# Kernel tuning notes

Hardware: AMD Instinct MI355X
Metric: run time of the kernel (lower is better)

The kernel has to match this reference:

```python
import jax, jax.numpy as jnp
import numpy as np

N = 12288
D = 16


def setup_inputs() -> dict:
    key = jax.random.key(0)
    k_a, k_u1, k_u2 = jax.random.split(key, 3)
    # 0/1 directed adjacency matrix (dense, as nx.to_numpy_array produces)
    A = jax.random.randint(k_a, (N, N), 0, 2).astype(jnp.float32)
    # tf.random.uniform init for the factor matrices
    U1 = jax.random.uniform(k_u1, (N, D), dtype=jnp.float32)
    U2 = jax.random.uniform(k_u2, (N, D), dtype=jnp.float32)
    lmbd1 = jnp.float32(0.01)
    return {"A": A, "U1": U1, "U2": U2, "lmbd1": lmbd1}


def reference(A, U1, U2, lmbd1):
    # scores[i,j] = <U1[i], U2[j]>  -> full N x N materialization (hot path)
    scores = U1 @ U2.T  # [N, N]
    # original: log(1 / (1 + exp(-scores))) == log_sigmoid(scores)
    loss = -jnp.sum(A * jax.nn.log_sigmoid(scores))
    # L1 regularization: sum over lmbd1*(|U1| + |U2|) elementwise
    loss = loss + lmbd1 * (jnp.sum(jnp.abs(U1)) + jnp.sum(jnp.abs(U2)))
    return loss
```

## Files before the change

### kernel.cpp

```cpp
#include <hip/hip_runtime.h>

#define N_DIM 12288
#define D_DIM 16
#define TILE  256
#define NTILE (N_DIM / TILE)

typedef float f4 __attribute__((ext_vector_type(4)));

__global__ void zero_kernel(float* __restrict__ out) {
    out[0] = 0.0f;
}

__global__ void l1_kernel(const float* __restrict__ U1,
                          const float* __restrict__ U2,
                          const float* __restrict__ lmbd,
                          float* __restrict__ out) {
    const int M = N_DIM * D_DIM;
    int idx = blockIdx.x * blockDim.x + threadIdx.x;
    int stride = gridDim.x * blockDim.x;
    float s = 0.0f;
    for (int i = idx; i < M; i += stride)
        s += fabsf(U1[i]) + fabsf(U2[i]);
    #pragma unroll
    for (int off = 32; off; off >>= 1)
        s += __shfl_down(s, off, 64);
    __shared__ float ws[4];
    int lane = threadIdx.x & 63;
    int wave = threadIdx.x >> 6;
    if (lane == 0) ws[wave] = s;
    __syncthreads();
    if (threadIdx.x == 0)
        atomicAdd(out, lmbd[0] * (ws[0] + ws[1] + ws[2] + ws[3]));
}

__global__ __launch_bounds__(256, 4)
void loss_kernel(const float* __restrict__ A,
                 const float* __restrict__ U1,
                 const float* __restrict__ U2,
                 float* __restrict__ ws) {
    const int t    = threadIdx.x;
    const int lane = t & 63;
    const int wave = t >> 6;
    const int r0   = blockIdx.y * TILE;
    const int c0   = blockIdx.x * TILE;

    float u2r[4][D_DIM];
    #pragma unroll
    for (int c = 0; c < 4; ++c) {
        const f4* p = (const f4*)(U2 + (size_t)(c0 + lane * 4 + c) * D_DIM);
        f4 qa = p[0], qb = p[1], qc = p[2], qd = p[3];
        u2r[c][0]  = qa.x; u2r[c][1]  = qa.y; u2r[c][2]  = qa.z; u2r[c][3]  = qa.w;
        u2r[c][4]  = qb.x; u2r[c][5]  = qb.y; u2r[c][6]  = qb.z; u2r[c][7]  = qb.w;
        u2r[c][8]  = qc.x; u2r[c][9]  = qc.y; u2r[c][10] = qc.z; u2r[c][11] = qc.w;
        u2r[c][12] = qd.x; u2r[c][13] = qd.y; u2r[c][14] = qd.z; u2r[c][15] = qd.w;
    }

    const int urow0 = __builtin_amdgcn_readfirstlane(r0 + wave * 64);
    const float* __restrict__ up = U1 + (size_t)urow0 * D_DIM;
    const float* __restrict__ ap =
        A + (size_t)(r0 + wave * 64) * N_DIM + (size_t)c0 + lane * 4;

    const float L2E = 1.4426950408889634f;
    float acc = 0.0f;

    f4 av[2], bv[2];

#define LOADG(buf, g)                                                          \
    { buf[0] = *(const f4*)(ap + (size_t)(2 * (g))     * N_DIM);               \
      buf[1] = *(const f4*)(ap + (size_t)(2 * (g) + 1) * N_DIM); }

#define COMPG(buf, g)                                                          \
    { float p0 = 1.0f, p1 = 1.0f, p2 = 1.0f, p3 = 1.0f;                        \
      _Pragma("unroll")                                                        \
      for (int r2 = 0; r2 < 2; ++r2) {                                         \
          const float* u = up + (size_t)(2 * (g) + r2) * D_DIM;                \
          float s0 = 0.f, s1 = 0.f, s2 = 0.f, s3 = 0.f;                        \
          _Pragma("unroll")                                                    \
          for (int k = 0; k < D_DIM; ++k) {                                    \
              float uk = u[k];                    \
              s0 = fmaf(uk, u2r[0][k], s0);                                    \
              s1 = fmaf(uk, u2r[1][k], s1);                                    \
              s2 = fmaf(uk, u2r[2][k], s2);                                    \
              s3 = fmaf(uk, u2r[3][k], s3);                                    \
          }                                                                    \
          float e0 = __builtin_amdgcn_exp2f(-L2E * s0);                        \
          float e1 = __builtin_amdgcn_exp2f(-L2E * s1);                        \
          float e2 = __builtin_amdgcn_exp2f(-L2E * s2);                        \
          float e3 = __builtin_amdgcn_exp2f(-L2E * s3);                        \
          f4 a = buf[r2];                                                      \
          p0 *= fmaf(a.x, e0, 1.0f);                                           \
          p1 *= fmaf(a.y, e1, 1.0f);                                           \
          p2 *= fmaf(a.z, e2, 1.0f);                                           \
          p3 *= fmaf(a.w, e3, 1.0f);                                           \
      }                                                                        \
      acc += __builtin_amdgcn_logf((p0 * p1) * (p2 * p3)); }

    LOADG(av, 0);
    #pragma unroll
    for (int gg = 0; gg < 16; ++gg) {
        LOADG(bv, 2 * gg + 1);
        COMPG(av, 2 * gg);
        if (gg < 15) LOADG(av, 2 * gg + 2);
        COMPG(bv, 2 * gg + 1);
    }
#undef LOADG
#undef COMPG

    float part = acc * 0.69314718055994531f;

    #pragma unroll
    for (int off = 32; off; off >>= 1)
        part += __shfl_down(part, off, 64);
    __shared__ float wsum[4];
    if (lane == 0) wsum[wave] = part;
    __syncthreads();
    if (t == 0)
        ws[blockIdx.y * NTILE + blockIdx.x] =
            wsum[0] + wsum[1] + wsum[2] + wsum[3];
}

__global__ void reduce_kernel(const float* __restrict__ ws,
                              float* __restrict__ out) {
    const int M = NTILE * NTILE;
    float s = 0.0f;
    for (int i = threadIdx.x; i < M; i += 256)
        s += ws[i];
    #pragma unroll
    for (int off = 32; off; off >>= 1)
        s += __shfl_down(s, off, 64);
    __shared__ float wsum[4];
    int lane = threadIdx.x & 63;
    int wave = threadIdx.x >> 6;
    if (lane == 0) wsum[wave] = s;
    __syncthreads();
    if (threadIdx.x == 0)
        atomicAdd(out, wsum[0] + wsum[1] + wsum[2] + wsum[3]);
}

extern "C" void kernel_launch(void* const* d_in, const int* in_sizes, int n_in,
                              void* d_out, int out_size, void* d_ws, size_t ws_size,
                              hipStream_t stream) {
    const float* A    = (const float*)d_in[0];
    const float* U1   = (const float*)d_in[1];
    const float* U2   = (const float*)d_in[2];
    const float* lmbd = (const float*)d_in[3];
    float* out = (float*)d_out;
    float* wsf = (float*)d_ws;

    zero_kernel<<<1, 64, 0, stream>>>(out);
    l1_kernel<<<256, 256, 0, stream>>>(U1, U2, lmbd, out);

    dim3 grid(NTILE, NTILE);
    loss_kernel<<<grid, 256, 0, stream>>>(A, U1, U2, wsf);
    reduce_kernel<<<1, 256, 0, stream>>>(wsf, out);
}
```

Baseline: 780.2 us.

## Pack adjacency matrix into a bitmap before the fused loss kernel

Adds a pre-pass that turns the float adjacency matrix into a 1-bit-per-entry bitmap by testing one exponent bit of each float. The loss kernel then stages its 256x256 bit tile in shared memory and decodes A per element, instead of streaming float4 loads through a software double buffer. The full A matrix is still read once per call, by the pack kernel, so this adds an extra launch and an 18 MB write and read-back. It also assumes every A entry is exactly 0.0 or 1.0, and the main loop is now only partially unrolled.

```diff
diff --git a/kernel.cpp b/kernel.cpp
--- a/kernel.cpp
+++ b/kernel.cpp
@@ -4,6 +4,8 @@
 #define D_DIM 16
 #define TILE  256
 #define NTILE (N_DIM / TILE)
+#define BM_BYTES ((size_t)N_DIM * N_DIM / 8)
+#define PART_OFF (32u << 20)
 
 typedef float f4 __attribute__((ext_vector_type(4)));
 
@@ -33,16 +35,42 @@
         atomicAdd(out, lmbd[0] * (ws[0] + ws[1] + ws[2] + ws[3]));
 }
 
+__global__ __launch_bounds__(256, 8)
+void pack_kernel(const float* __restrict__ A, unsigned char* __restrict__ bm) {
+    size_t idx = (size_t)blockIdx.x * blockDim.x + threadIdx.x;
+    size_t stride = (size_t)gridDim.x * blockDim.x;
+    #pragma unroll 4
+    for (size_t b = idx; b < BM_BYTES; b += stride) {
+        const uint4* p = (const uint4*)(A + b * 8);
+        uint4 x = p[0], y = p[1];
+        unsigned v =  ((x.x >> 29) & 1u)        | (((x.y >> 29) & 1u) << 1)
+                   | (((x.z >> 29) & 1u) << 2)  | (((x.w >> 29) & 1u) << 3)
+                   | (((y.x >> 29) & 1u) << 4)  | (((y.y >> 29) & 1u) << 5)
+                   | (((y.z >> 29) & 1u) << 6)  | (((y.w >> 29) & 1u) << 7);
+        bm[b] = (unsigned char)v;
+    }
+}
+
 __global__ __launch_bounds__(256, 4)
-void loss_kernel(const float* __restrict__ A,
+void loss_kernel(const unsigned char* __restrict__ bm,
                  const float* __restrict__ U1,
                  const float* __restrict__ U2,
-                 float* __restrict__ ws) {
+                 float* __restrict__ partials) {
     const int t    = threadIdx.x;
     const int lane = t & 63;
     const int wave = t >> 6;
     const int r0   = blockIdx.y * TILE;
     const int c0   = blockIdx.x * TILE;
+
+    __shared__ unsigned char bmt[TILE * (TILE / 8)];
+
+    {
+        const uint4* src = (const uint4*)(bm + (size_t)(r0 + t) * (N_DIM / 8)
+                                             + (size_t)(c0 / 8));
+        uint4* dst = (uint4*)(bmt + t * 32);
+        dst[0] = src[0];
+        dst[1] = src[1];
+    }
 
     float u2r[4][D_DIM];
     #pragma unroll
@@ -55,56 +83,47 @@
         u2r[c][12] = qd.x; u2r[c][13] = qd.y; u2r[c][14] = qd.z; u2r[c][15] = qd.w;
     }
 
+    __syncthreads();
+
     const int urow0 = __builtin_amdgcn_readfirstlane(r0 + wave * 64);
     const float* __restrict__ up = U1 + (size_t)urow0 * D_DIM;
-    const float* __restrict__ ap =
-        A + (size_t)(r0 + wave * 64) * N_DIM + (size_t)c0 + lane * 4;
 
     const float L2E = 1.4426950408889634f;
     float acc = 0.0f;
 
-    f4 av[2], bv[2];
-
-#define LOADG(buf, g)                                                          \
-    { buf[0] = *(const f4*)(ap + (size_t)(2 * (g))     * N_DIM);               \
-      buf[1] = *(const f4*)(ap + (size_t)(2 * (g) + 1) * N_DIM); }
-
-#define COMPG(buf, g)                                                          \
-    { float p0 = 1.0f, p1 = 1.0f, p2 = 1.0f, p3 = 1.0f;                        \
-      _Pragma("unroll")                                                        \
-      for (int r2 = 0; r2 < 2; ++r2) {                                         \
-          const float* u = up + (size_t)(2 * (g) + r2) * D_DIM;                \
-          float s0 = 0.f, s1 = 0.f, s2 = 0.f, s3 = 0.f;                        \
-          _Pragma("unroll")                                                    \
-          for (int k = 0; k < D_DIM; ++k) {                                    \
-              float uk = u[k];                    \
-              s0 = fmaf(uk, u2r[0][k], s0);                                    \
-              s1 = fmaf(uk, u2r[1][k], s1);                                    \
-              s2 = fmaf(uk, u2r[2][k], s2);                                    \
-              s3 = fmaf(uk, u2r[3][k], s3);                                    \
-          }                                                                    \
-          float e0 = __builtin_amdgcn_exp2f(-L2E * s0);                        \
-          float e1 = __builtin_amdgcn_exp2f(-L2E * s1);                        \
-          float e2 = __builtin_amdgcn_exp2f(-L2E * s2);                        \
-          float e3 = __builtin_amdgcn_exp2f(-L2E * s3);                        \
-          f4 a = buf[r2];                                                      \
-          p0 *= fmaf(a.x, e0, 1.0f);                                           \
-          p1 *= fmaf(a.y, e1, 1.0f);                                           \
-          p2 *= fmaf(a.z, e2, 1.0f);                                           \
-          p3 *= fmaf(a.w, e3, 1.0f);                                           \
-      }                                                                        \
-      acc += __builtin_amdgcn_logf((p0 * p1) * (p2 * p3)); }
-
-    LOADG(av, 0);
-    #pragma unroll
-    for (int gg = 0; gg < 16; ++gg) {
-        LOADG(bv, 2 * gg + 1);
-        COMPG(av, 2 * gg);
-        if (gg < 15) LOADG(av, 2 * gg + 2);
-        COMPG(bv, 2 * gg + 1);
+    #pragma unroll 2
+    for (int g = 0; g < 32; ++g) {
+        float p0 = 1.0f, p1 = 1.0f, p2 = 1.0f, p3 = 1.0f;
+        #pragma unroll
+        for (int r2 = 0; r2 < 2; ++r2) {
+            const int lrow = wave * 64 + 2 * g + r2;
+            const float* u = up + (size_t)(2 * g + r2) * D_DIM;
+            float s0 = 0.f, s1 = 0.f, s2 = 0.f, s3 = 0.f;
+            #pragma unroll
+            for (int k = 0; k < D_DIM; ++k) {
+                float uk = u[k];
+                s0 = fmaf(uk, u2r[0][k], s0);
+                s1 = fmaf(uk, u2r[1][k], s1);
+                s2 = fmaf(uk, u2r[2][k], s2);
+                s3 = fmaf(uk, u2r[3][k], s3);
+            }
+            float e0 = __builtin_amdgcn_exp2f(-L2E * s0);
+            float e1 = __builtin_amdgcn_exp2f(-L2E * s1);
+            float e2 = __builtin_amdgcn_exp2f(-L2E * s2);
+            float e3 = __builtin_amdgcn_exp2f(-L2E * s3);
+            unsigned b8  = bmt[lrow * 32 + (lane >> 1)];
+            unsigned nib = b8 >> ((lane & 1) * 4);
+            float a0 = (float)( nib       & 1u);
+            float a1 = (float)((nib >> 1) & 1u);
+            float a2 = (float)((nib >> 2) & 1u);
+            float a3 = (float)((nib >> 3) & 1u);
+            p0 *= fmaf(a0, e0, 1.0f);
+            p1 *= fmaf(a1, e1, 1.0f);
+            p2 *= fmaf(a2, e2, 1.0f);
+            p3 *= fmaf(a3, e3, 1.0f);
+        }
+        acc += __builtin_amdgcn_logf((p0 * p1) * (p2 * p3));
     }
-#undef LOADG
-#undef COMPG
 
     float part = acc * 0.69314718055994531f;
 
@@ -115,16 +134,16 @@
     if (lane == 0) wsum[wave] = part;
     __syncthreads();
     if (t == 0)
-        ws[blockIdx.y * NTILE + blockIdx.x] =
+        partials[blockIdx.y * NTILE + blockIdx.x] =
             wsum[0] + wsum[1] + wsum[2] + wsum[3];
 }
 
-__global__ void reduce_kernel(const float* __restrict__ ws,
+__global__ void reduce_kernel(const float* __restrict__ partials,
                               float* __restrict__ out) {
     const int M = NTILE * NTILE;
     float s = 0.0f;
     for (int i = threadIdx.x; i < M; i += 256)
-        s += ws[i];
+        s += partials[i];
     #pragma unroll
     for (int off = 32; off; off >>= 1)
         s += __shfl_down(s, off, 64);
@@ -145,12 +164,15 @@
     const float* U2   = (const float*)d_in[2];
     const float* lmbd = (const float*)d_in[3];
     float* out = (float*)d_out;
-    float* wsf = (float*)d_ws;
+    unsigned char* bm = (unsigned char*)d_ws;
+    float* partials   = (float*)((char*)d_ws + PART_OFF);
 
     zero_kernel<<<1, 64, 0, stream>>>(out);
     l1_kernel<<<256, 256, 0, stream>>>(U1, U2, lmbd, out);
 
+    pack_kernel<<<2048, 256, 0, stream>>>(A, bm);
+
     dim3 grid(NTILE, NTILE);
-    loss_kernel<<<grid, 256, 0, stream>>>(A, U1, U2, wsf);
-    reduce_kernel<<<1, 256, 0, stream>>>(wsf, out);
+    loss_kernel<<<grid, 256, 0, stream>>>(bm, U1, U2, partials);
+    reduce_kernel<<<1, 256, 0, stream>>>(partials, out);
 }
```

Result: slower. 889.1 us (+14.0%).
